# Optimization experiments

Measured on AMD Instinct MI355X. Metric: run time of the kernel, lower is better.

The kernel has to match this reference:

```python
import jax, jax.numpy as jnp
import numpy as np

TEMP = 0.1  # temperature from __init__
EPS = 1e-8  # torch CosineSimilarity eps
B, C, D = 64, 32, 256


def _cos(a, b):
    # a, b: [..., F] -> [...]; matches torch: dot / max(|a||b|, eps)
    dot = jnp.sum(a * b, axis=-1)
    na = jnp.linalg.norm(a, axis=-1)
    nb = jnp.linalg.norm(b, axis=-1)
    return dot / jnp.maximum(na * nb, EPS)


def setup_inputs() -> dict:
    key = jax.random.key(0)
    k1, k2, k3, k4 = jax.random.split(key, 4)
    children_is = jax.random.normal(k1, (B, C, D), dtype=jnp.float32)
    children_js = jax.random.normal(k2, (B, C, D), dtype=jnp.float32)
    neg_idx_j = jax.random.randint(k3, (B, B, C), 0, C, dtype=jnp.int32)
    neg_idx_k = jax.random.randint(k4, (B, B, C), 0, C, dtype=jnp.int32)
    partnet_ids = jnp.arange(B, dtype=jnp.int64)
    return {"children_is": children_is, "children_js": children_js,
            "neg_idx_j": neg_idx_j, "neg_idx_k": neg_idx_k,
            "partnet_ids": partnet_ids}


def reference(children_is, children_js, neg_idx_j, neg_idx_k, partnet_ids):
    b, c, d = children_is.shape
    flat_i = children_is.reshape(b, c * d)          # anchors [B, C*D]
    flat_j = children_js.reshape(b, c * d)

    # positive: anchor i vs children_js[i]
    pos = _cos(flat_i, flat_j) / TEMP               # [B]

    src = jnp.arange(b)[None, :, None]              # [1, B, 1]
    # negatives gathered from children_js: [B, B, C, D] -> [B, B, C*D]
    g_j = children_js[src, neg_idx_j].reshape(b, b, c * d)
    # negatives gathered from children_is
    g_k = children_is[src, neg_idx_k].reshape(b, b, c * d)

    sim_j = _cos(flat_i[:, None, :], g_j) / TEMP    # [B, B]
    sim_k = _cos(flat_i[:, None, :], g_k) / TEMP    # [B, B]

    eye = jnp.eye(b, dtype=bool)
    neg_inf = jnp.asarray(-jnp.inf, sim_j.dtype)
    sim_j = jnp.where(eye, neg_inf, sim_j)          # drop j == i
    sim_k = jnp.where(eye, neg_inf, sim_k)          # drop k == i

    # CrossEntropy(reduction='sum') with label 0 per anchor:
    # loss_i = -pos_i + logsumexp([pos_i, negatives...])
    logits = jnp.concatenate([pos[:, None], sim_j, sim_k], axis=1)  # [B, 1+2B]
    lse = jax.scipy.special.logsumexp(logits, axis=1)
    loss = jnp.sum(lse - pos)
    return loss / (2 * b)
```

## Files before the change

kernel.cpp:

```cpp
#include <hip/hip_runtime.h>
#include <math.h>

#define BB 64
#define CC 32
#define DD 256
#define TEMP 0.1f
#define EPSC 1e-8f

typedef const __attribute__((address_space(1))) unsigned int* gptr_u32;
typedef __attribute__((address_space(3))) unsigned int* lptr_u32;

__device__ __forceinline__ float wave_reduce_sum(float v) {
    #pragma unroll
    for (int off = 32; off > 0; off >>= 1)
        v += __shfl_down(v, off, 64);
    return v;
}

__global__ __launch_bounds__(256) void sim_part_kernel(
        const float* __restrict__ xis,
        const float* __restrict__ xjs,
        const int* __restrict__ idxj,
        const int* __restrict__ idxk,
        float* __restrict__ pos,
        float* __restrict__ part)
{
    __shared__ float sj[CC * DD];
    __shared__ float sk[CC * DD];

    const int m = blockIdx.x;
    const int lane = threadIdx.x & 63;
    const int wave = __builtin_amdgcn_readfirstlane(threadIdx.x >> 6);

    {
        const float* gj = xjs + (size_t)m * CC * DD;
        const float* gi = xis + (size_t)m * CC * DD;
        #pragma unroll
        for (int k = 0; k < 8; ++k) {
            const int off = (threadIdx.x + k * 256) * 4;
            __builtin_amdgcn_global_load_lds((gptr_u32)(gj + off), (lptr_u32)(sj + off), 16, 0, 0);
            __builtin_amdgcn_global_load_lds((gptr_u32)(gi + off), (lptr_u32)(sk + off), 16, 0, 0);
        }
    }
    __syncthreads();

    const int ibase = blockIdx.y * 8 + wave * 2;

    #pragma unroll
    for (int ii = 0; ii < 2; ++ii) {
        const int i = ibase + ii;
        const bool diag = (i == m);
        const int* __restrict__ pj = idxj + ((size_t)i * BB + m) * CC;
        const int* __restrict__ pk = idxk + ((size_t)i * BB + m) * CC;
        const float4* a4 = (const float4*)(xis + (size_t)i * CC * DD);

        float dj = 0.f, dk = 0.f, naa = 0.f, njj = 0.f, nkk = 0.f;
        #pragma unroll 8
        for (int c = 0; c < CC; ++c) {
            const int ij = diag ? c : pj[c];
            const int ik = diag ? c : pk[c];
            float4 a  = a4[c * (DD / 4) + lane];
            float4 jv = ((const float4*)(sj + ij * DD))[lane];
            float4 kv = ((const float4*)(sk + ik * DD))[lane];
            dj  += a.x * jv.x + a.y * jv.y + a.z * jv.z + a.w * jv.w;
            dk  += a.x * kv.x + a.y * kv.y + a.z * kv.z + a.w * kv.w;
            naa += a.x * a.x  + a.y * a.y  + a.z * a.z  + a.w * a.w;
            njj += jv.x * jv.x + jv.y * jv.y + jv.z * jv.z + jv.w * jv.w;
            nkk += kv.x * kv.x + kv.y * kv.y + kv.z * kv.z + kv.w * kv.w;
        }
        dj  = wave_reduce_sum(dj);
        dk  = wave_reduce_sum(dk);
        naa = wave_reduce_sum(naa);
        njj = wave_reduce_sum(njj);
        nkk = wave_reduce_sum(nkk);

        if (lane == 0) {
            const float ni = sqrtf(naa);
            if (diag) {
                pos[i] = dj / fmaxf(ni * sqrtf(njj), EPSC) / TEMP;
                part[m * BB + i] = 0.0f;
            } else {
                const float s1 = dj / fmaxf(ni * sqrtf(njj), EPSC) / TEMP;
                const float s2 = dk / fmaxf(ni * sqrtf(nkk), EPSC) / TEMP;
                part[m * BB + i] = expf(s1 - 10.0f) + expf(s2 - 10.0f);
            }
        }
    }
}

__global__ __launch_bounds__(256) void loss_kernel(
        const float* __restrict__ pos,
        const float* __restrict__ part,
        float* __restrict__ out)
{
    __shared__ float sp[4][BB];
    const int t = threadIdx.x;
    const int i = t & 63;
    const int q = t >> 6;

    float s = 0.f;
    #pragma unroll
    for (int mm = 0; mm < 16; ++mm)
        s += part[(q * 16 + mm) * BB + i];
    sp[q][i] = s;
    __syncthreads();

    if (t < 64) {
        const float p = pos[i];
        const float tot = sp[0][i] + sp[1][i] + sp[2][i] + sp[3][i] + expf(p - 10.0f);
        float v = 10.0f + logf(tot) - p;
        v = wave_reduce_sum(v);
        if (i == 0) out[0] = v * (1.0f / (2.0f * BB));
    }
}

extern "C" void kernel_launch(void* const* d_in, const int* in_sizes, int n_in,
                              void* d_out, int out_size, void* d_ws, size_t ws_size,
                              hipStream_t stream) {
    const float* xis  = (const float*)d_in[0];
    const float* xjs  = (const float*)d_in[1];
    const int*   idxj = (const int*)d_in[2];
    const int*   idxk = (const int*)d_in[3];
    float* out = (float*)d_out;

    float* ws   = (float*)d_ws;
    float* pos  = ws;
    float* part = pos + BB;

    sim_part_kernel<<<dim3(BB, 8), 256, 0, stream>>>(xis, xjs, idxj, idxk, pos, part);
    loss_kernel<<<1, 256, 0, stream>>>(pos, part, out);
}
```

Measured before the change: 77.76 us.

## Precompute per-row LDS norms and use one wave per anchor row

Each block now computes the squared norm of every child row of xjs[m] and xis[m] once into shared memory. The dot-product loop then only accumulates the two dot products and the anchor norm, and the negative norms are gathered from that table by index and reduced with a shuffle. Blocks grow to 512 threads with one anchor row per wave instead of two, which doubles the wave count per block. The shared-memory footprint is unchanged at about 64KB, so occupancy depends on LDS limits, and the added norm pass plus a second barrier cost extra work up front.

```diff
diff --git a/kernel.cpp b/kernel.cpp
--- a/kernel.cpp
+++ b/kernel.cpp
@@ -17,7 +17,7 @@
     return v;
 }
 
-__global__ __launch_bounds__(256) void sim_part_kernel(
+__global__ __launch_bounds__(512, 4) void sim_part_kernel(
         const float* __restrict__ xis,
         const float* __restrict__ xjs,
         const int* __restrict__ idxj,
@@ -27,6 +27,7 @@
 {
     __shared__ float sj[CC * DD];
     __shared__ float sk[CC * DD];
+    __shared__ float ssn[2 * CC];
 
     const int m = blockIdx.x;
     const int lane = threadIdx.x & 63;
@@ -36,54 +37,74 @@
         const float* gj = xjs + (size_t)m * CC * DD;
         const float* gi = xis + (size_t)m * CC * DD;
         #pragma unroll
-        for (int k = 0; k < 8; ++k) {
-            const int off = (threadIdx.x + k * 256) * 4;
+        for (int k = 0; k < 4; ++k) {
+            const int off = (threadIdx.x + k * 512) * 4;
             __builtin_amdgcn_global_load_lds((gptr_u32)(gj + off), (lptr_u32)(sj + off), 16, 0, 0);
             __builtin_amdgcn_global_load_lds((gptr_u32)(gi + off), (lptr_u32)(sk + off), 16, 0, 0);
         }
     }
     __syncthreads();
 
-    const int ibase = blockIdx.y * 8 + wave * 2;
+    #pragma unroll
+    for (int t = 0; t < 8; ++t) {
+        const int r = wave * 8 + t;
+        const float* base = (r < CC) ? (sj + r * DD) : (sk + (r - CC) * DD);
+        const float4 v = ((const float4*)base)[lane];
+        float s = v.x * v.x + v.y * v.y + v.z * v.z + v.w * v.w;
+        s = wave_reduce_sum(s);
+        if (lane == 0) ssn[r] = s;
+    }
+    __syncthreads();
 
+    const int i = blockIdx.y * 8 + wave;
+    const bool diag = (i == m);
+    const int* __restrict__ pj = idxj + ((size_t)i * BB + m) * CC;
+    const int* __restrict__ pk = idxk + ((size_t)i * BB + m) * CC;
+    const float4* a4 = (const float4*)(xis + (size_t)i * CC * DD);
+
+    float dj = 0.f, dk = 0.f, naa = 0.f;
+    #pragma unroll 4
+    for (int c = 0; c < CC; ++c) {
+        const int ij = diag ? c : pj[c];
+        const int ik = diag ? c : pk[c];
+        const float4 a  = a4[c * (DD / 4) + lane];
+        const float4 jv = ((const float4*)(sj + ij * DD))[lane];
+        const float4 kv = ((const float4*)(sk + ik * DD))[lane];
+        dj  += a.x * jv.x + a.y * jv.y + a.z * jv.z + a.w * jv.w;
+        dk  += a.x * kv.x + a.y * kv.y + a.z * kv.z + a.w * kv.w;
+        naa += a.x * a.x  + a.y * a.y  + a.z * a.z  + a.w * a.w;
+    }
     #pragma unroll
-    for (int ii = 0; ii < 2; ++ii) {
-        const int i = ibase + ii;
-        const bool diag = (i == m);
-        const int* __restrict__ pj = idxj + ((size_t)i * BB + m) * CC;
-        const int* __restrict__ pk = idxk + ((size_t)i * BB + m) * CC;
-        const float4* a4 = (const float4*)(xis + (size_t)i * CC * DD);
+    for (int off = 32; off > 0; off >>= 1) {
+        dj  += __shfl_down(dj,  off, 64);
+        dk  += __shfl_down(dk,  off, 64);
+        naa += __shfl_down(naa, off, 64);
+    }
 
-        float dj = 0.f, dk = 0.f, naa = 0.f, njj = 0.f, nkk = 0.f;
-        #pragma unroll 8
-        for (int c = 0; c < CC; ++c) {
-            const int ij = diag ? c : pj[c];
-            const int ik = diag ? c : pk[c];
-            float4 a  = a4[c * (DD / 4) + lane];
-            float4 jv = ((const float4*)(sj + ij * DD))[lane];
-            float4 kv = ((const float4*)(sk + ik * DD))[lane];
-            dj  += a.x * jv.x + a.y * jv.y + a.z * jv.z + a.w * jv.w;
-            dk  += a.x * kv.x + a.y * kv.y + a.z * kv.z + a.w * kv.w;
-            naa += a.x * a.x  + a.y * a.y  + a.z * a.z  + a.w * a.w;
-            njj += jv.x * jv.x + jv.y * jv.y + jv.z * jv.z + jv.w * jv.w;
-            nkk += kv.x * kv.x + kv.y * kv.y + kv.z * kv.z + kv.w * kv.w;
-        }
-        dj  = wave_reduce_sum(dj);
-        dk  = wave_reduce_sum(dk);
-        naa = wave_reduce_sum(naa);
-        njj = wave_reduce_sum(njj);
-        nkk = wave_reduce_sum(nkk);
+    const int l2 = lane & 31;
+    int row;
+    if (diag) {
+        row = l2;
+    } else {
+        const int* pb = (lane < 32) ? pj : pk;
+        row = pb[l2];
+    }
+    float nv = ssn[(lane < 32 ? 0 : CC) + row];
+    #pragma unroll
+    for (int off = 16; off > 0; off >>= 1)
+        nv += __shfl_down(nv, off, 64);
+    const float njj = __shfl(nv, 0, 64);
+    const float nkk = __shfl(nv, 32, 64);
 
-        if (lane == 0) {
-            const float ni = sqrtf(naa);
-            if (diag) {
-                pos[i] = dj / fmaxf(ni * sqrtf(njj), EPSC) / TEMP;
-                part[m * BB + i] = 0.0f;
-            } else {
-                const float s1 = dj / fmaxf(ni * sqrtf(njj), EPSC) / TEMP;
-                const float s2 = dk / fmaxf(ni * sqrtf(nkk), EPSC) / TEMP;
-                part[m * BB + i] = expf(s1 - 10.0f) + expf(s2 - 10.0f);
-            }
+    if (lane == 0) {
+        const float ni = sqrtf(naa);
+        if (diag) {
+            pos[i] = dj / fmaxf(ni * sqrtf(njj), EPSC) / TEMP;
+            part[m * BB + i] = 0.0f;
+        } else {
+            const float s1 = dj / fmaxf(ni * sqrtf(njj), EPSC) / TEMP;
+            const float s2 = dk / fmaxf(ni * sqrtf(nkk), EPSC) / TEMP;
+            part[m * BB + i] = expf(s1 - 10.0f) + expf(s2 - 10.0f);
         }
     }
 }
@@ -127,6 +148,6 @@
     float* pos  = ws;
     float* part = pos + BB;
 
-    sim_part_kernel<<<dim3(BB, 8), 256, 0, stream>>>(xis, xjs, idxj, idxk, pos, part);
+    sim_part_kernel<<<dim3(BB, 8), 512, 0, stream>>>(xis, xjs, idxj, idxk, pos, part);
     loss_kernel<<<1, 256, 0, stream>>>(pos, part, out);
 }
```

New measurement: 76.89 us. About the same (-1.1%).
